# Optimization experiments

Hardware: AMD Instinct MI355X
Metric: run time of the kernel (lower is better)

Reference implementation:

```python
import jax, jax.numpy as jnp
import numpy as np

B, R, S = 4, 65536, 48  # batch, rays (256x256), depth_resolution


def setup_inputs() -> dict:
    key = jax.random.key(0)
    k1, k2, k3 = jax.random.split(key, 3)
    colors = jax.random.uniform(k1, (B, R, S, 3), dtype=jnp.float32)
    densities = jax.random.normal(k2, (B, R, S, 1), dtype=jnp.float32)
    # stratified depths in [-1, 1], monotone along sample axis (axis=-2)
    depths = jnp.sort(
        jax.random.uniform(k3, (B, R, S, 1), dtype=jnp.float32) * 2.0 - 1.0,
        axis=-2,
    )
    return {"colors": colors, "densities": densities, "depths": depths}


def reference(colors, densities, depths):
    # MipRayMarcher2.run_forward
    deltas = depths[:, :, 1:] - depths[:, :, :-1]                     # [B,R,S-1,1]
    colors_mid = (colors[:, :, :-1] + colors[:, :, 1:]) * 0.5         # [B,R,S-1,3]
    densities_mid = (densities[:, :, :-1] + densities[:, :, 1:]) * 0.5
    depths_mid = (depths[:, :, :-1] + depths[:, :, 1:]) * 0.5

    densities_mid = jax.nn.softplus(densities_mid - 1.0)
    density_delta = densities_mid * deltas
    alpha = 1.0 - jnp.exp(-density_delta)                             # [B,R,S-1,1]

    # exclusive cumulative transmittance along the sample axis
    alpha_shifted = jnp.concatenate(
        [jnp.ones_like(alpha[:, :, :1]), 1.0 - alpha + 1e-10], axis=-2
    )
    weights = alpha * jnp.cumprod(alpha_shifted, axis=-2)[:, :, :-1]  # [B,R,S-1,1]

    composite_rgb = jnp.sum(weights * colors_mid, axis=-2)            # [B,R,3]
    weight_total = jnp.sum(weights, axis=2)                           # [B,R,1]
    composite_depth = jnp.sum(weights * depths_mid, axis=-2) / weight_total
    composite_depth = jnp.nan_to_num(composite_depth, nan=jnp.inf)
    composite_depth = jnp.clip(composite_depth, jnp.min(depths), jnp.max(depths))

    composite_rgb = composite_rgb * 2.0 - 1.0
    return composite_rgb, composite_depth, weights
```

## Files before the change

kernel.cpp:

```cpp
#include <hip/hip_runtime.h>
#include <math.h>


#define S_SAMPLES 48
#define S_INTERVALS 47
#define WR 16
#define RSTRIDE 52
#define BT 64
#define WAVE_LDS (2 * WR * RSTRIDE)

__global__ __launch_bounds__(BT, 3) void raymarch_kernel(
    const float* __restrict__ colors,
    const float* __restrict__ densities,
    const float* __restrict__ depths,
    float* __restrict__ out_rgb,
    float* __restrict__ out_depth,
    float* __restrict__ out_w,
    int nRays) {
    __shared__ float4 smem4[WAVE_LDS / 4];
    const int lane = threadIdx.x;
    float* A = (float*)smem4;
    float* B = A + WR * RSTRIDE;

    const int waveId = blockIdx.x;
    const size_t wray = (size_t)waveId * WR;

    const int r = lane >> 2;
    const int q = lane & 3;

    const float* gdepf = depths + wray * S_SAMPLES;
    const float* gdenf = densities + wray * S_SAMPLES;
    const int mbase = 12 * lane;
    const int offD = (q < 3) ? 12 : 11;
    float4 dA = *(const float4*)&gdepf[mbase];
    float4 dB4 = *(const float4*)&gdepf[mbase + 4];
    float4 dC = *(const float4*)&gdepf[mbase + 8];
    float dD = gdepf[mbase + offD];
    float4 nA = *(const float4*)&gdenf[mbase];
    float4 nB4 = *(const float4*)&gdenf[mbase + 4];
    float4 nC = *(const float4*)&gdenf[mbase + 8];
    float nD = gdenf[mbase + offD];

    const float4* gcol4 = (const float4*)(colors + wray * (S_SAMPLES * 3));
    const int rr0 = lane / 12, i40 = lane - rr0 * 12;
    const int f1 = lane + 64, rr1 = f1 / 12, i41 = f1 - rr1 * 12;
    const int f2 = lane + 128, rr2 = f2 / 12, i42 = f2 - rr2 * 12;
    float4 u0 = gcol4[rr0 * 36 + i40];
    float4 u1 = gcol4[rr1 * 36 + i41];
    float4 u2 = gcol4[rr2 * 36 + i42];
    float4 u3 = gcol4[rr0 * 36 + 12 + i40];
    float4 u4 = gcol4[rr1 * 36 + 12 + i41];
    float4 u5 = gcol4[rr2 * 36 + 12 + i42];
    float4 u6 = gcol4[rr0 * 36 + 24 + i40];
    float4 u7 = gcol4[rr1 * 36 + 24 + i41];
    float4 u8 = gcol4[rr2 * 36 + 24 + i42];

    const int rbase = r * RSTRIDE;
    const int base = rbase + 12 * q;
    const float LOG2E = 1.4426950408889634f;

    float g0, g1, g2, g3, g4, g5, g6, g7, g8, g9, g10, g11;
#define DD(dP, dN, nP, nN, OUT, HAS)                                   \
    do {                                                               \
        float xs = (0.5f * ((nP) + (nN)) - 1.f) * LOG2E;               \
        float sp2 = fmaxf(xs, 0.f) + log2f(1.f + exp2f(-fabsf(xs)));   \
        OUT = (HAS) ? ((dN) - (dP)) * sp2 : 0.f;                       \
    } while (0)
    DD(dA.x, dA.y, nA.x, nA.y, g0, true);
    DD(dA.y, dA.z, nA.y, nA.z, g1, true);
    DD(dA.z, dA.w, nA.z, nA.w, g2, true);
    DD(dA.w, dB4.x, nA.w, nB4.x, g3, true);
    DD(dB4.x, dB4.y, nB4.x, nB4.y, g4, true);
    DD(dB4.y, dB4.z, nB4.y, nB4.z, g5, true);
    DD(dB4.z, dB4.w, nB4.z, nB4.w, g6, true);
    DD(dB4.w, dC.x, nB4.w, nC.x, g7, true);
    DD(dC.x, dC.y, nC.x, nC.y, g8, true);
    DD(dC.y, dC.z, nC.y, nC.z, g9, true);
    DD(dC.z, dC.w, nC.z, nC.w, g10, true);
    DD(dC.w, dD, nC.w, nD, g11, (q < 3));
#undef DD

    float S1 = g0, S2 = S1 + g1, S3 = S2 + g2, S4 = S3 + g3;
    float S5 = S4 + g4, S6 = S5 + g5, S7 = S6 + g6, S8 = S7 + g7;
    float S9 = S8 + g8, S10 = S9 + g9, S11 = S10 + g10, S12 = S11 + g11;

    float Sloc = S12;
    float u1s = __shfl_up(Sloc, 1);
    float ps = (q >= 1) ? Sloc + u1s : Sloc;
    float u2s = __shfl_up(ps, 2);
    float incl = (q >= 2) ? ps + u2s : ps;
    float u3s = __shfl_up(incl, 1);
    float Sexc = (q >= 1) ? u3s : 0.f;

    float Tp = exp2f(-Sexc);
    float T1 = exp2f(-(Sexc + S1)), T2 = exp2f(-(Sexc + S2));
    float T3 = exp2f(-(Sexc + S3)), T4 = exp2f(-(Sexc + S4));
    float T5 = exp2f(-(Sexc + S5)), T6 = exp2f(-(Sexc + S6));
    float T7 = exp2f(-(Sexc + S7)), T8 = exp2f(-(Sexc + S8));
    float T9 = exp2f(-(Sexc + S9)), T10 = exp2f(-(Sexc + S10));
    float T11 = exp2f(-(Sexc + S11)), T12 = exp2f(-(Sexc + S12));
    float W0 = Tp - T1, W1 = T1 - T2, W2 = T2 - T3, W3 = T3 - T4;
    float W4 = T4 - T5, W5 = T5 - T6, W6 = T6 - T7, W7 = T7 - T8;
    float W8 = T8 - T9, W9 = T9 - T10, W10 = T10 - T11, W11 = T11 - T12;

    float ad = 0.f;
    ad = fmaf(W0, 0.5f * (dA.x + dA.y), ad);
    ad = fmaf(W1, 0.5f * (dA.y + dA.z), ad);
    ad = fmaf(W2, 0.5f * (dA.z + dA.w), ad);
    ad = fmaf(W3, 0.5f * (dA.w + dB4.x), ad);
    ad = fmaf(W4, 0.5f * (dB4.x + dB4.y), ad);
    ad = fmaf(W5, 0.5f * (dB4.y + dB4.z), ad);
    ad = fmaf(W6, 0.5f * (dB4.z + dB4.w), ad);
    ad = fmaf(W7, 0.5f * (dB4.w + dC.x), ad);
    ad = fmaf(W8, 0.5f * (dC.x + dC.y), ad);
    ad = fmaf(W9, 0.5f * (dC.y + dC.z), ad);
    ad = fmaf(W10, 0.5f * (dC.z + dC.w), ad);
    ad = fmaf(W11, 0.5f * (dC.w + dD), ad);
    float aw = Tp - T12;

    *(float4*)&A[base + 0] = make_float4(W0, W1, W2, W3);
    *(float4*)&A[base + 4] = make_float4(W4, W5, W6, W7);
    *(float4*)&A[base + 8] = make_float4(W8, W9, W10, W11);

#pragma unroll
    for (int off = 1; off <= 2; off <<= 1) {
        aw += __shfl_xor(aw, off);
        ad += __shfl_xor(ad, off);
    }
    float lastDep = __shfl(dC.w, lane | 3);
    float firstDep = __shfl(dA.x, lane & ~3);
    if (q == 0) {
        float d = ad / aw;
        d = fminf(fmaxf(d, firstDep), lastDep);
        out_depth[wray + r] = d;
    }

    asm volatile("" : "+v"(u0.x), "+v"(u0.y), "+v"(u0.z), "+v"(u0.w),
                      "+v"(u1.x), "+v"(u1.y), "+v"(u1.z), "+v"(u1.w),
                      "+v"(u2.x), "+v"(u2.y), "+v"(u2.z), "+v"(u2.w),
                      "+v"(u3.x), "+v"(u3.y), "+v"(u3.z), "+v"(u3.w));
    asm volatile("" : "+v"(u4.x), "+v"(u4.y), "+v"(u4.z), "+v"(u4.w),
                      "+v"(u5.x), "+v"(u5.y), "+v"(u5.z), "+v"(u5.w),
                      "+v"(u6.x), "+v"(u6.y), "+v"(u6.z), "+v"(u6.w),
                      "+v"(u7.x), "+v"(u7.y), "+v"(u7.z), "+v"(u7.w),
                      "+v"(u8.x), "+v"(u8.y), "+v"(u8.z), "+v"(u8.w));

    float Wm1 = __shfl_up(W11, 1);
    if (q == 0) Wm1 = 0.f;
    float v0 = 0.5f * (Wm1 + W0), v1 = 0.5f * (W0 + W1);
    float v2 = 0.5f * (W1 + W2), v3 = 0.5f * (W2 + W3);
    float v4 = 0.5f * (W3 + W4), v5 = 0.5f * (W4 + W5);
    float v6 = 0.5f * (W5 + W6), v7 = 0.5f * (W6 + W7);
    float v8 = 0.5f * (W7 + W8), v9 = 0.5f * (W8 + W9);
    float v10 = 0.5f * (W9 + W10), v11 = 0.5f * (W10 + W11);

    asm volatile("" ::: "memory");

    {
        float* gw = out_w + wray * S_INTERVALS;
#pragma unroll
        for (int k = 0; k < 12; ++k) {
            int g = lane + k * 64;
            if (g < WR * S_INTERVALS) {
                int ray = g / S_INTERVALS;
                int s = g - ray * S_INTERVALS;
                gw[g] = A[ray * RSTRIDE + s];
            }
        }
    }

    float a0 = 0.f, a1 = 0.f, a2 = 0.f;

#define ACC4(vA, vB, vC, vD, fa, fb, fc)                                \
    do {                                                                \
        a0 = fmaf(vA, (fa).x, a0); a1 = fmaf(vA, (fa).y, a1);           \
        a2 = fmaf(vA, (fa).z, a2); a0 = fmaf(vB, (fa).w, a0);           \
        a1 = fmaf(vB, (fb).x, a1); a2 = fmaf(vB, (fb).y, a2);           \
        a0 = fmaf(vC, (fb).z, a0); a1 = fmaf(vC, (fb).w, a1);           \
        a2 = fmaf(vC, (fc).x, a2); a0 = fmaf(vD, (fc).y, a0);           \
        a1 = fmaf(vD, (fc).z, a1); a2 = fmaf(vD, (fc).w, a2);           \
    } while (0)
#define LD3(f, loc)                                                     \
    float4 f##a = *(const float4*)&B[rbase + (loc)];                    \
    float4 f##b = *(const float4*)&B[rbase + (loc) + 4];                \
    float4 f##c = *(const float4*)&B[rbase + (loc) + 8];
#define STAGE(pa, pb, pc)                                               \
    do {                                                                \
        *(float4*)&B[rr0 * RSTRIDE + i40 * 4] = pa;                     \
        *(float4*)&B[rr1 * RSTRIDE + i41 * 4] = pb;                     \
        *(float4*)&B[rr2 * RSTRIDE + i42 * 4] = pc;                     \
    } while (0)

    STAGE(u0, u1, u2);
    asm volatile("" ::: "memory");
    if (q == 0) {
        LD3(x, 0) LD3(y, 12) LD3(z, 24)
        ACC4(v0, v1, v2, v3, xa, xb, xc);
        ACC4(v4, v5, v6, v7, ya, yb, yc);
        ACC4(v8, v9, v10, v11, za, zb, zc);
    } else if (q == 1) {
        LD3(x, 36)
        ACC4(v0, v1, v2, v3, xa, xb, xc);
    }
    asm volatile("" ::: "memory");
    STAGE(u3, u4, u5);
    asm volatile("" ::: "memory");
    if (q == 1) {
        LD3(x, 0) LD3(y, 12)
        ACC4(v4, v5, v6, v7, xa, xb, xc);
        ACC4(v8, v9, v10, v11, ya, yb, yc);
    } else if (q == 2) {
        LD3(x, 24) LD3(y, 36)
        ACC4(v0, v1, v2, v3, xa, xb, xc);
        ACC4(v4, v5, v6, v7, ya, yb, yc);
    }
    asm volatile("" ::: "memory");
    STAGE(u6, u7, u8);
    asm volatile("" ::: "memory");
    if (q == 2) {
        LD3(x, 0)
        ACC4(v8, v9, v10, v11, xa, xb, xc);
    } else if (q == 3) {
        LD3(x, 12) LD3(y, 24) LD3(z, 36)
        ACC4(v0, v1, v2, v3, xa, xb, xc);
        ACC4(v4, v5, v6, v7, ya, yb, yc);
        ACC4(v8, v9, v10, v11, za, zb, zc);
    }
#undef STAGE
#undef LD3
#undef ACC4

#pragma unroll
    for (int off = 1; off <= 2; off <<= 1) {
        a0 += __shfl_xor(a0, off);
        a1 += __shfl_xor(a1, off);
        a2 += __shfl_xor(a2, off);
    }
    if (q == 0) {
        size_t rb = (wray + r) * 3;
        out_rgb[rb + 0] = fmaf(a0, 2.f, -1.f);
        out_rgb[rb + 1] = fmaf(a1, 2.f, -1.f);
        out_rgb[rb + 2] = fmaf(a2, 2.f, -1.f);
    }
}

extern "C" void kernel_launch(void* const* d_in, const int* in_sizes, int n_in,
                              void* d_out, int out_size, void* d_ws, size_t ws_size,
                              hipStream_t stream) {
    const float* colors = (const float*)d_in[0];
    const float* densities = (const float*)d_in[1];
    const float* depths = (const float*)d_in[2];

    const int nRays = in_sizes[2] / S_SAMPLES;
    const int nWaves = nRays / WR;

    float* out = (float*)d_out;
    float* out_rgb = out;
    float* out_depth = out + (size_t)nRays * 3;
    float* out_w = out + (size_t)nRays * 4;

    raymarch_kernel<<<nWaves, BT, 0, stream>>>(
        colors, densities, depths, out_rgb, out_depth, out_w, nRays);
}
```

Measured before the change: 53.12 us.

## Make each wave persistent over groups with register double-buffered prefetch

Each single-wave block now processes 8 consecutive 16-ray groups instead of one. It prefetches the next group's depths, densities and colors into a second register set while computing the current group, so global load latency overlaps with compute. Inline asm pins keep the prefetched registers live. The cost is a doubled register footprint, with launch bounds lowered to 2 waves per EU, and 8x fewer blocks. That could reduce occupancy-based latency hiding and leave a smaller grid to balance across CUs.

```diff
diff --git a/kernel.cpp b/kernel.cpp
--- a/kernel.cpp
+++ b/kernel.cpp
@@ -7,56 +7,78 @@
 #define WR 16
 #define RSTRIDE 52
 #define BT 64
+#define GPB 8
 #define WAVE_LDS (2 * WR * RSTRIDE)
 
-__global__ __launch_bounds__(BT, 3) void raymarch_kernel(
-    const float* __restrict__ colors,
-    const float* __restrict__ densities,
-    const float* __restrict__ depths,
-    float* __restrict__ out_rgb,
-    float* __restrict__ out_depth,
-    float* __restrict__ out_w,
-    int nRays) {
-    __shared__ float4 smem4[WAVE_LDS / 4];
-    const int lane = threadIdx.x;
-    float* A = (float*)smem4;
-    float* B = A + WR * RSTRIDE;
-
-    const int waveId = blockIdx.x;
-    const size_t wray = (size_t)waveId * WR;
-
-    const int r = lane >> 2;
-    const int q = lane & 3;
-
-    const float* gdepf = depths + wray * S_SAMPLES;
-    const float* gdenf = densities + wray * S_SAMPLES;
-    const int mbase = 12 * lane;
-    const int offD = (q < 3) ? 12 : 11;
-    float4 dA = *(const float4*)&gdepf[mbase];
-    float4 dB4 = *(const float4*)&gdepf[mbase + 4];
-    float4 dC = *(const float4*)&gdepf[mbase + 8];
-    float dD = gdepf[mbase + offD];
-    float4 nA = *(const float4*)&gdenf[mbase];
-    float4 nB4 = *(const float4*)&gdenf[mbase + 4];
-    float4 nC = *(const float4*)&gdenf[mbase + 8];
-    float nD = gdenf[mbase + offD];
-
-    const float4* gcol4 = (const float4*)(colors + wray * (S_SAMPLES * 3));
-    const int rr0 = lane / 12, i40 = lane - rr0 * 12;
-    const int f1 = lane + 64, rr1 = f1 / 12, i41 = f1 - rr1 * 12;
-    const int f2 = lane + 128, rr2 = f2 / 12, i42 = f2 - rr2 * 12;
-    float4 u0 = gcol4[rr0 * 36 + i40];
-    float4 u1 = gcol4[rr1 * 36 + i41];
-    float4 u2 = gcol4[rr2 * 36 + i42];
-    float4 u3 = gcol4[rr0 * 36 + 12 + i40];
-    float4 u4 = gcol4[rr1 * 36 + 12 + i41];
-    float4 u5 = gcol4[rr2 * 36 + 12 + i42];
-    float4 u6 = gcol4[rr0 * 36 + 24 + i40];
-    float4 u7 = gcol4[rr1 * 36 + 24 + i41];
-    float4 u8 = gcol4[rr2 * 36 + 24 + i42];
-
-    const int rbase = r * RSTRIDE;
-    const int base = rbase + 12 * q;
+struct Grp {
+    float4 dA, dB4, dC, nA, nB4, nC;
+    float dD, nD;
+    float4 u0, u1, u2, u3, u4, u5, u6, u7, u8;
+};
+
+struct LaneCtx {
+    int lane, r, q, rbase, base, mbase, offD;
+    int rc0, rc1, rc2;
+    int b0, b1, b2;
+    float* A;
+    float* B;
+};
+
+__device__ __forceinline__ void load_grp(Grp& S, const LaneCtx& L,
+                                         const float* __restrict__ depths,
+                                         const float* __restrict__ densities,
+                                         const float* __restrict__ colors,
+                                         int grp) {
+    const float* gdepf = depths + (size_t)grp * (WR * S_SAMPLES);
+    const float* gdenf = densities + (size_t)grp * (WR * S_SAMPLES);
+    const float4* gcol4 = (const float4*)(colors + (size_t)grp * (WR * S_SAMPLES * 3));
+    S.dA = *(const float4*)&gdepf[L.mbase];
+    S.dB4 = *(const float4*)&gdepf[L.mbase + 4];
+    S.dC = *(const float4*)&gdepf[L.mbase + 8];
+    S.dD = gdepf[L.mbase + L.offD];
+    S.nA = *(const float4*)&gdenf[L.mbase];
+    S.nB4 = *(const float4*)&gdenf[L.mbase + 4];
+    S.nC = *(const float4*)&gdenf[L.mbase + 8];
+    S.nD = gdenf[L.mbase + L.offD];
+    S.u0 = gcol4[L.rc0];
+    S.u1 = gcol4[L.rc1];
+    S.u2 = gcol4[L.rc2];
+    S.u3 = gcol4[L.rc0 + 12];
+    S.u4 = gcol4[L.rc1 + 12];
+    S.u5 = gcol4[L.rc2 + 12];
+    S.u6 = gcol4[L.rc0 + 24];
+    S.u7 = gcol4[L.rc1 + 24];
+    S.u8 = gcol4[L.rc2 + 24];
+}
+
+__device__ __forceinline__ void pin_grp(Grp& S) {
+    asm volatile("" : "+v"(S.dA.x), "+v"(S.dA.y), "+v"(S.dA.z), "+v"(S.dA.w),
+                      "+v"(S.dB4.x), "+v"(S.dB4.y), "+v"(S.dB4.z), "+v"(S.dB4.w),
+                      "+v"(S.dC.x), "+v"(S.dC.y), "+v"(S.dC.z), "+v"(S.dC.w),
+                      "+v"(S.dD), "+v"(S.nD));
+    asm volatile("" : "+v"(S.nA.x), "+v"(S.nA.y), "+v"(S.nA.z), "+v"(S.nA.w),
+                      "+v"(S.nB4.x), "+v"(S.nB4.y), "+v"(S.nB4.z), "+v"(S.nB4.w),
+                      "+v"(S.nC.x), "+v"(S.nC.y), "+v"(S.nC.z), "+v"(S.nC.w));
+    asm volatile("" : "+v"(S.u0.x), "+v"(S.u0.y), "+v"(S.u0.z), "+v"(S.u0.w),
+                      "+v"(S.u1.x), "+v"(S.u1.y), "+v"(S.u1.z), "+v"(S.u1.w),
+                      "+v"(S.u2.x), "+v"(S.u2.y), "+v"(S.u2.z), "+v"(S.u2.w),
+                      "+v"(S.u3.x), "+v"(S.u3.y), "+v"(S.u3.z), "+v"(S.u3.w));
+    asm volatile("" : "+v"(S.u4.x), "+v"(S.u4.y), "+v"(S.u4.z), "+v"(S.u4.w),
+                      "+v"(S.u5.x), "+v"(S.u5.y), "+v"(S.u5.z), "+v"(S.u5.w),
+                      "+v"(S.u6.x), "+v"(S.u6.y), "+v"(S.u6.z), "+v"(S.u6.w),
+                      "+v"(S.u7.x), "+v"(S.u7.y), "+v"(S.u7.z), "+v"(S.u7.w));
+    asm volatile("" : "+v"(S.u8.x), "+v"(S.u8.y), "+v"(S.u8.z), "+v"(S.u8.w));
+}
+
+__device__ __forceinline__ void compute_grp(
+    Grp& S, const LaneCtx& L, int grp,
+    float* __restrict__ out_rgb, float* __restrict__ out_depth,
+    float* __restrict__ out_w) {
+    const size_t wray = (size_t)grp * WR;
+    const int lane = L.lane, q = L.q, r = L.r;
+    const int rbase = L.rbase, base = L.base;
+    float* A = L.A;
+    float* B = L.B;
     const float LOG2E = 1.4426950408889634f;
 
     float g0, g1, g2, g3, g4, g5, g6, g7, g8, g9, g10, g11;
@@ -66,18 +88,18 @@
         float sp2 = fmaxf(xs, 0.f) + log2f(1.f + exp2f(-fabsf(xs)));   \
         OUT = (HAS) ? ((dN) - (dP)) * sp2 : 0.f;                       \
     } while (0)
-    DD(dA.x, dA.y, nA.x, nA.y, g0, true);
-    DD(dA.y, dA.z, nA.y, nA.z, g1, true);
-    DD(dA.z, dA.w, nA.z, nA.w, g2, true);
-    DD(dA.w, dB4.x, nA.w, nB4.x, g3, true);
-    DD(dB4.x, dB4.y, nB4.x, nB4.y, g4, true);
-    DD(dB4.y, dB4.z, nB4.y, nB4.z, g5, true);
-    DD(dB4.z, dB4.w, nB4.z, nB4.w, g6, true);
-    DD(dB4.w, dC.x, nB4.w, nC.x, g7, true);
-    DD(dC.x, dC.y, nC.x, nC.y, g8, true);
-    DD(dC.y, dC.z, nC.y, nC.z, g9, true);
-    DD(dC.z, dC.w, nC.z, nC.w, g10, true);
-    DD(dC.w, dD, nC.w, nD, g11, (q < 3));
+    DD(S.dA.x, S.dA.y, S.nA.x, S.nA.y, g0, true);
+    DD(S.dA.y, S.dA.z, S.nA.y, S.nA.z, g1, true);
+    DD(S.dA.z, S.dA.w, S.nA.z, S.nA.w, g2, true);
+    DD(S.dA.w, S.dB4.x, S.nA.w, S.nB4.x, g3, true);
+    DD(S.dB4.x, S.dB4.y, S.nB4.x, S.nB4.y, g4, true);
+    DD(S.dB4.y, S.dB4.z, S.nB4.y, S.nB4.z, g5, true);
+    DD(S.dB4.z, S.dB4.w, S.nB4.z, S.nB4.w, g6, true);
+    DD(S.dB4.w, S.dC.x, S.nB4.w, S.nC.x, g7, true);
+    DD(S.dC.x, S.dC.y, S.nC.x, S.nC.y, g8, true);
+    DD(S.dC.y, S.dC.z, S.nC.y, S.nC.z, g9, true);
+    DD(S.dC.z, S.dC.w, S.nC.z, S.nC.w, g10, true);
+    DD(S.dC.w, S.dD, S.nC.w, S.nD, g11, (q < 3));
 #undef DD
 
     float S1 = g0, S2 = S1 + g1, S3 = S2 + g2, S4 = S3 + g3;
@@ -104,18 +126,18 @@
     float W8 = T8 - T9, W9 = T9 - T10, W10 = T10 - T11, W11 = T11 - T12;
 
     float ad = 0.f;
-    ad = fmaf(W0, 0.5f * (dA.x + dA.y), ad);
-    ad = fmaf(W1, 0.5f * (dA.y + dA.z), ad);
-    ad = fmaf(W2, 0.5f * (dA.z + dA.w), ad);
-    ad = fmaf(W3, 0.5f * (dA.w + dB4.x), ad);
-    ad = fmaf(W4, 0.5f * (dB4.x + dB4.y), ad);
-    ad = fmaf(W5, 0.5f * (dB4.y + dB4.z), ad);
-    ad = fmaf(W6, 0.5f * (dB4.z + dB4.w), ad);
-    ad = fmaf(W7, 0.5f * (dB4.w + dC.x), ad);
-    ad = fmaf(W8, 0.5f * (dC.x + dC.y), ad);
-    ad = fmaf(W9, 0.5f * (dC.y + dC.z), ad);
-    ad = fmaf(W10, 0.5f * (dC.z + dC.w), ad);
-    ad = fmaf(W11, 0.5f * (dC.w + dD), ad);
+    ad = fmaf(W0, 0.5f * (S.dA.x + S.dA.y), ad);
+    ad = fmaf(W1, 0.5f * (S.dA.y + S.dA.z), ad);
+    ad = fmaf(W2, 0.5f * (S.dA.z + S.dA.w), ad);
+    ad = fmaf(W3, 0.5f * (S.dA.w + S.dB4.x), ad);
+    ad = fmaf(W4, 0.5f * (S.dB4.x + S.dB4.y), ad);
+    ad = fmaf(W5, 0.5f * (S.dB4.y + S.dB4.z), ad);
+    ad = fmaf(W6, 0.5f * (S.dB4.z + S.dB4.w), ad);
+    ad = fmaf(W7, 0.5f * (S.dB4.w + S.dC.x), ad);
+    ad = fmaf(W8, 0.5f * (S.dC.x + S.dC.y), ad);
+    ad = fmaf(W9, 0.5f * (S.dC.y + S.dC.z), ad);
+    ad = fmaf(W10, 0.5f * (S.dC.z + S.dC.w), ad);
+    ad = fmaf(W11, 0.5f * (S.dC.w + S.dD), ad);
     float aw = Tp - T12;
 
     *(float4*)&A[base + 0] = make_float4(W0, W1, W2, W3);
@@ -127,23 +149,13 @@
         aw += __shfl_xor(aw, off);
         ad += __shfl_xor(ad, off);
     }
-    float lastDep = __shfl(dC.w, lane | 3);
-    float firstDep = __shfl(dA.x, lane & ~3);
+    float lastDep = __shfl(S.dC.w, lane | 3);
+    float firstDep = __shfl(S.dA.x, lane & ~3);
     if (q == 0) {
         float d = ad / aw;
         d = fminf(fmaxf(d, firstDep), lastDep);
         out_depth[wray + r] = d;
     }
-
-    asm volatile("" : "+v"(u0.x), "+v"(u0.y), "+v"(u0.z), "+v"(u0.w),
-                      "+v"(u1.x), "+v"(u1.y), "+v"(u1.z), "+v"(u1.w),
-                      "+v"(u2.x), "+v"(u2.y), "+v"(u2.z), "+v"(u2.w),
-                      "+v"(u3.x), "+v"(u3.y), "+v"(u3.z), "+v"(u3.w));
-    asm volatile("" : "+v"(u4.x), "+v"(u4.y), "+v"(u4.z), "+v"(u4.w),
-                      "+v"(u5.x), "+v"(u5.y), "+v"(u5.z), "+v"(u5.w),
-                      "+v"(u6.x), "+v"(u6.y), "+v"(u6.z), "+v"(u6.w),
-                      "+v"(u7.x), "+v"(u7.y), "+v"(u7.z), "+v"(u7.w),
-                      "+v"(u8.x), "+v"(u8.y), "+v"(u8.z), "+v"(u8.w));
 
     float Wm1 = __shfl_up(W11, 1);
     if (q == 0) Wm1 = 0.f;
@@ -170,7 +182,6 @@
     }
 
     float a0 = 0.f, a1 = 0.f, a2 = 0.f;
-
 #define ACC4(vA, vB, vC, vD, fa, fb, fc)                                \
     do {                                                                \
         a0 = fmaf(vA, (fa).x, a0); a1 = fmaf(vA, (fa).y, a1);           \
@@ -186,12 +197,13 @@
     float4 f##c = *(const float4*)&B[rbase + (loc) + 8];
 #define STAGE(pa, pb, pc)                                               \
     do {                                                                \
-        *(float4*)&B[rr0 * RSTRIDE + i40 * 4] = pa;                     \
-        *(float4*)&B[rr1 * RSTRIDE + i41 * 4] = pb;                     \
-        *(float4*)&B[rr2 * RSTRIDE + i42 * 4] = pc;                     \
+        *(float4*)&B[L.b0] = pa;                                        \
+        *(float4*)&B[L.b1] = pb;                                        \
+        *(float4*)&B[L.b2] = pc;                                        \
     } while (0)
 
-    STAGE(u0, u1, u2);
+    asm volatile("" ::: "memory");
+    STAGE(S.u0, S.u1, S.u2);
     asm volatile("" ::: "memory");
     if (q == 0) {
         LD3(x, 0) LD3(y, 12) LD3(z, 24)
@@ -203,7 +215,7 @@
         ACC4(v0, v1, v2, v3, xa, xb, xc);
     }
     asm volatile("" ::: "memory");
-    STAGE(u3, u4, u5);
+    STAGE(S.u3, S.u4, S.u5);
     asm volatile("" ::: "memory");
     if (q == 1) {
         LD3(x, 0) LD3(y, 12)
@@ -215,7 +227,7 @@
         ACC4(v4, v5, v6, v7, ya, yb, yc);
     }
     asm volatile("" ::: "memory");
-    STAGE(u6, u7, u8);
+    STAGE(S.u6, S.u7, S.u8);
     asm volatile("" ::: "memory");
     if (q == 2) {
         LD3(x, 0)
@@ -244,6 +256,54 @@
     }
 }
 
+__global__ __launch_bounds__(BT, 2) void raymarch_kernel(
+    const float* __restrict__ colors,
+    const float* __restrict__ densities,
+    const float* __restrict__ depths,
+    float* __restrict__ out_rgb,
+    float* __restrict__ out_depth,
+    float* __restrict__ out_w,
+    int nRays) {
+    __shared__ float4 smem4[WAVE_LDS / 4];
+    LaneCtx L;
+    L.lane = threadIdx.x;
+    L.r = L.lane >> 2;
+    L.q = L.lane & 3;
+    L.rbase = L.r * RSTRIDE;
+    L.base = L.rbase + 12 * L.q;
+    L.mbase = 12 * L.lane;
+    L.offD = (L.q < 3) ? 12 : 11;
+    {
+        int rr0 = L.lane / 12, i40 = L.lane - rr0 * 12;
+        int f1 = L.lane + 64, rr1 = f1 / 12, i41 = f1 - rr1 * 12;
+        int f2 = L.lane + 128, rr2 = f2 / 12, i42 = f2 - rr2 * 12;
+        L.rc0 = rr0 * 36 + i40;
+        L.rc1 = rr1 * 36 + i41;
+        L.rc2 = rr2 * 36 + i42;
+        L.b0 = rr0 * RSTRIDE + i40 * 4;
+        L.b1 = rr1 * RSTRIDE + i41 * 4;
+        L.b2 = rr2 * RSTRIDE + i42 * 4;
+    }
+    L.A = (float*)smem4;
+    L.B = L.A + WR * RSTRIDE;
+
+    const int gbase = blockIdx.x * GPB;
+
+    Grp sA, sB;
+    load_grp(sA, L, depths, densities, colors, gbase);
+
+#pragma unroll
+    for (int ii = 0; ii < GPB / 2; ++ii) {
+        load_grp(sB, L, depths, densities, colors, gbase + 2 * ii + 1);
+        compute_grp(sA, L, gbase + 2 * ii, out_rgb, out_depth, out_w);
+        pin_grp(sB);
+        if (ii < GPB / 2 - 1)
+            load_grp(sA, L, depths, densities, colors, gbase + 2 * ii + 2);
+        compute_grp(sB, L, gbase + 2 * ii + 1, out_rgb, out_depth, out_w);
+        if (ii < GPB / 2 - 1) pin_grp(sA);
+    }
+}
+
 extern "C" void kernel_launch(void* const* d_in, const int* in_sizes, int n_in,
                               void* d_out, int out_size, void* d_ws, size_t ws_size,
                               hipStream_t stream) {
@@ -252,13 +312,14 @@
     const float* depths = (const float*)d_in[2];
 
     const int nRays = in_sizes[2] / S_SAMPLES;
-    const int nWaves = nRays / WR;
+    const int nGroups = nRays / WR;
+    const int nBlocks = nGroups / GPB;
 
     float* out = (float*)d_out;
     float* out_rgb = out;
     float* out_depth = out + (size_t)nRays * 3;
     float* out_w = out + (size_t)nRays * 4;
 
-    raymarch_kernel<<<nWaves, BT, 0, stream>>>(
+    raymarch_kernel<<<nBlocks, BT, 0, stream>>>(
         colors, densities, depths, out_rgb, out_depth, out_w, nRays);
 }
```

New measurement: 61.23 us. +15.3%, slower.
